# Optimization experiments

Hardware: AMD Instinct MI355X
Metric: run time of the kernel (lower is better)

## Reference

```python
import jax, jax.numpy as jnp
from jax import lax
import numpy as np

B, L, H, V = 256, 2048, 128, 32000
THR = 0.4      # energy_threshold
LN_EPS = 1e-5  # torch LayerNorm default


def setup_inputs() -> dict:
    key = jax.random.key(0)
    ks = jax.random.split(key, 12)
    s = lambda k, shp, scale: (jax.random.normal(k, shp, dtype=jnp.float32) * scale)
    return {
        "seq": jax.random.randint(ks[0], (B, L), 0, V),
        "embed": s(ks[1], (V, H), 0.02),
        "W1": s(ks[2], (H, 2 * H), H ** -0.5),
        "b1": jnp.zeros((2 * H,), jnp.float32),
        "W2": s(ks[3], (2 * H, H), (2 * H) ** -0.5),
        "b2": jnp.zeros((H,), jnp.float32),
        "gamma": jnp.ones((H,), jnp.float32),
        "beta": jnp.zeros((H,), jnp.float32),
        "Wrp": s(ks[4], (H, H), H ** -0.5),
        "brp": jnp.zeros((H,), jnp.float32),
        "Wout": s(ks[5], (H, V), H ** -0.5),
        "bout": jnp.zeros((V,), jnp.float32),
    }


def _encode(seq, embed, W1, b1, W2, b2, gamma, beta):
    e = embed[seq]                                         # [B,L,H]
    ff = jnp.maximum(e @ W1 + b1, 0.0) @ W2 + b2           # [B,L,H]
    y = e + ff
    mu = y.mean(-1, keepdims=True)
    var = ((y - mu) ** 2).mean(-1, keepdims=True)
    return (y - mu) * lax.rsqrt(var + LN_EPS) * gamma + beta


def reference(seq, embed, W1, b1, W2, b2, gamma, beta, Wrp, brp, Wout, bout):
    h_all = _encode(seq, embed, W1, b1, W2, b2, gamma, beta)  # [B,L,H]

    def step(M, k):
        # k = v = h_all[:, t, :]  -> [B,H]
        v = k
        vp = jnp.einsum('bij,bj->bi', M, k)
        error = v - vp / (jnp.sum(k * k, axis=-1, keepdims=True) + 1e-6)
        gate = (jnp.linalg.norm(error, axis=-1)
                > THR * jnp.linalg.norm(v, axis=-1)).astype(M.dtype)  # [B]
        M = M + gate[:, None, None] * jnp.einsum('bi,bj->bij', error, k)
        return M, None

    M0 = jnp.zeros((B, H, H), h_all.dtype)
    ks = jnp.swapaxes(h_all[:, :-1, :], 0, 1)               # [L-1,B,H]
    M_fin, _ = lax.scan(step, M0, ks)
    r = jnp.einsum('bij,bj->bi', M_fin, h_all[:, -1, :])    # [B,H]
    return (r @ Wrp + brp) @ Wout + bout                    # [B,V]
```

## Files before the change

kernel.cpp:

```cpp
#include <hip/hip_runtime.h>
#include <hip/hip_bf16.h>


#define BB 256
#define LL 2048
#define HH 128
#define VV 32000
#define RS 136

typedef float f32x2 __attribute__((ext_vector_type(2)));

__device__ __forceinline__ void dma16(const float* g, float* l) {
  __builtin_amdgcn_global_load_lds(
      (const __attribute__((address_space(1))) void*)g,
      (__attribute__((address_space(3))) void*)l,
      16, 0, 0);
}

template <int CTRL>
__device__ __forceinline__ float dppadd(float x) {
  int y = __builtin_amdgcn_update_dpp(0, __float_as_int(x), CTRL, 0xF, 0xF, true);
  return x + __int_as_float(y);
}

__device__ __forceinline__ void pkfma(f32x2& d, f32x2 a, f32x2 b) {
  asm("v_pk_fma_f32 %0, %1, %2, %0" : "+v"(d) : "v"(a), "v"(b));
}

__device__ __forceinline__ void barrier_lgkm() {
  asm volatile("s_waitcnt lgkmcnt(0)\n\ts_barrier" ::: "memory");
}
__device__ __forceinline__ void wait_vmN(int n) {
  if (n == 3)      asm volatile("s_waitcnt vmcnt(3)" ::: "memory");
  else if (n == 2) asm volatile("s_waitcnt vmcnt(2)" ::: "memory");
  else if (n == 1) asm volatile("s_waitcnt vmcnt(1)" ::: "memory");
  else             asm volatile("s_waitcnt vmcnt(0)" ::: "memory");
}

__global__ __launch_bounds__(256, 1) void build_htab_kernel(
    const float* __restrict__ embed,
    const float* __restrict__ W1,
    const float* __restrict__ b1,
    const float* __restrict__ W2,
    const float* __restrict__ b2,
    const float* __restrict__ gamma,
    const float* __restrict__ beta,
    float* __restrict__ Htab2)
{
  const int tid = threadIdx.x;
  const int j   = tid & 127;
  const int h2  = tid >> 7;

  float w1r[128];
#pragma unroll
  for (int m = 0; m < 128; ++m) w1r[m] = W1[m * 256 + tid];

  const float b1n = b1[tid];
  const float b2j = b2[j];
  const float gj  = gamma[j];
  const float bj  = beta[j];

  __shared__ __align__(16) float4 w2q[64][128];
  __shared__ __align__(16) float e_s[128];
  __shared__ __align__(16) float a_s[256];
  __shared__ float p_s[2][128];
  __shared__ float red[8];

  for (int idx = tid; idx < 8192; idx += 256) {
    int n4 = idx >> 7, jj = idx & 127;
    float4 w;
    w.x = W2[(size_t)(4 * n4 + 0) * 128 + jj];
    w.y = W2[(size_t)(4 * n4 + 1) * 128 + jj];
    w.z = W2[(size_t)(4 * n4 + 2) * 128 + jj];
    w.w = W2[(size_t)(4 * n4 + 3) * 128 + jj];
    w2q[n4][jj] = w;
  }
  __syncthreads();

  for (int v = blockIdx.x; v < VV; v += gridDim.x) {
    if (tid < 128) e_s[tid] = embed[(size_t)v * 128 + tid];
    __syncthreads();

    float acc[4] = {b1n, 0.f, 0.f, 0.f};
#pragma unroll
    for (int q = 0; q < 32; ++q) {
      float4 ev = *(const float4*)&e_s[4 * q];
      float t = ev.x * w1r[4 * q + 0];
      t = fmaf(ev.y, w1r[4 * q + 1], t);
      t = fmaf(ev.z, w1r[4 * q + 2], t);
      t = fmaf(ev.w, w1r[4 * q + 3], t);
      acc[q & 3] += t;
    }
    float a = fmaxf((acc[0] + acc[1]) + (acc[2] + acc[3]), 0.0f);
    a_s[tid] = a;
    __syncthreads();

    float p0 = 0.f, p1 = 0.f, p2v = 0.f, p3 = 0.f;
#pragma unroll
    for (int q = 0; q < 32; ++q) {
      int n4 = h2 * 32 + q;
      float4 av = *(const float4*)&a_s[4 * n4];
      float4 wq = w2q[n4][j];
      p0 = fmaf(av.x, wq.x, p0);
      p1 = fmaf(av.y, wq.y, p1);
      p2v = fmaf(av.z, wq.z, p2v);
      p3 = fmaf(av.w, wq.w, p3);
    }
    p_s[h2][j] = (p0 + p1) + (p2v + p3);
    __syncthreads();

    float y = 0.0f;
    if (tid < 128) {
      float ff = p_s[0][tid] + p_s[1][tid] + b2j;
      y = e_s[tid] + ff;
    }
    float s1 = y, s2 = y * y;
    s1 = dppadd<0xB1>(s1);  s2 = dppadd<0xB1>(s2);
    s1 = dppadd<0x4E>(s1);  s2 = dppadd<0x4E>(s2);
    s1 = dppadd<0x141>(s1); s2 = dppadd<0x141>(s2);
    s1 = dppadd<0x140>(s1); s2 = dppadd<0x140>(s2);
    s1 = dppadd<0x142>(s1); s2 = dppadd<0x142>(s2);
    s1 = dppadd<0x143>(s1); s2 = dppadd<0x143>(s2);
    if (tid < 128 && (tid & 63) == 63) {
      red[tid >> 6] = s1;
      red[2 + (tid >> 6)] = s2;
    }
    __syncthreads();
    float mu = (red[0] + red[1]) * (1.0f / 128.0f);
    float ms = (red[2] + red[3]) * (1.0f / 128.0f);
    float var = ms - mu * mu;
    float hv = 0.0f;
    if (tid < 128) {
      float dy = y - mu;
      hv = dy * (1.0f / sqrtf(var + 1e-5f)) * gj + bj;
      int ofs = tid + ((tid >> 6) << 2);
      Htab2[(size_t)v * RS + ofs] = hv;
    }
    float q2 = hv * hv;
    q2 = dppadd<0xB1>(q2);
    q2 = dppadd<0x4E>(q2);
    q2 = dppadd<0x141>(q2);
    q2 = dppadd<0x140>(q2);
    q2 = dppadd<0x142>(q2);
    q2 = dppadd<0x143>(q2);
    if (tid < 128 && (tid & 63) == 63) red[4 + (tid >> 6)] = q2;
    __syncthreads();
    if (tid == 0) {
      float kk = red[4] + red[5];
      Htab2[(size_t)v * RS + 132] = kk;
      Htab2[(size_t)v * RS + 133] = 1.0f / (kk + 1e-6f);
    }
    __syncthreads();
  }
}

__global__ __launch_bounds__(512, 2) void scan_kernel(
    const int* __restrict__ seq,
    const float* __restrict__ Htab2,
    const float* __restrict__ Wrp,
    const float* __restrict__ brp,
    float* __restrict__ rr)
{
  const int b     = blockIdx.x;
  const int tid   = threadIdx.x;
  const int i     = tid >> 2;
  const int q     = tid & 3;
  const int lane  = tid & 63;
  const int wv    = tid >> 6;
  const int iofs  = i + ((i >> 6) << 2);
  const int kbase = (q & 1) * 32 + (q >> 1) * 68;

  __shared__ int seq_s[LL];
  __shared__ __align__(16) float slots[8][RS];
  __shared__ __align__(16) float red_s[4][8];
  __shared__ __align__(16) float r_s[128];
  __shared__ float p2_s[4][128];

  {
    int t0 = seq[(size_t)b * LL + 0];
    int t1 = seq[(size_t)b * LL + 1];
    int t2 = seq[(size_t)b * LL + 2];
    int t3 = seq[(size_t)b * LL + 3];
    if (lane < 34) {
      dma16(Htab2 + (size_t)t0 * RS + lane * 4, &slots[0][0]);
      dma16(Htab2 + (size_t)t1 * RS + lane * 4, &slots[1][0]);
      dma16(Htab2 + (size_t)t2 * RS + lane * 4, &slots[2][0]);
      dma16(Htab2 + (size_t)t3 * RS + lane * 4, &slots[3][0]);
    }
  }
  for (int t = tid; t < LL; t += 512) seq_s[t] = seq[(size_t)b * LL + t];
  __syncthreads();

  f32x2 M2[16];
#pragma unroll
  for (int m = 0; m < 16; ++m) M2[m] = f32x2{0.f, 0.f};

  f32x2 kA[16], kB[16];
  float kiA, kkA, invA, kiB, kkB, invB;
  {
    const float4* kp = (const float4*)&slots[0][kbase];
#pragma unroll
    for (int m = 0; m < 8; ++m) {
      float4 tq = kp[m];
      kA[2 * m]     = f32x2{tq.x, tq.y};
      kA[2 * m + 1] = f32x2{tq.z, tq.w};
    }
    kiA = slots[0][iofs];
    float2 kv = *(const float2*)&slots[0][132];
    kkA = kv.x; invA = kv.y;
#pragma unroll
    for (int m = 0; m < 16; ++m) asm volatile("" : "+v"(kA[m]));
    asm volatile("" : "+v"(kiA), "+v"(kkA), "+v"(invA));
  }

  auto step = [&](f32x2 (&kc)[16], float ki_c, float kk_c, float inv_c,
                  f32x2 (&kn)[16], float& ki_n, float& kk_n, float& inv_n,
                  int t, int p, int sn, int sd, int nwait) {
    if (nwait == 3) {
      int tk = seq_s[t + 4];
      if (lane < 34)
        dma16(Htab2 + (size_t)tk * RS + lane * 4, &slots[sd][0]);
    }
    f32x2 a0{0.f,0.f}, a1{0.f,0.f}, a2{0.f,0.f}, a3{0.f,0.f};
#pragma unroll
    for (int m = 0; m < 4; ++m) {
      pkfma(a0, kc[4 * m + 0], M2[4 * m + 0]);
      pkfma(a1, kc[4 * m + 1], M2[4 * m + 1]);
      pkfma(a2, kc[4 * m + 2], M2[4 * m + 2]);
      pkfma(a3, kc[4 * m + 3], M2[4 * m + 3]);
    }
    float vp = ((a0.x + a0.y) + (a1.x + a1.y)) + ((a2.x + a2.y) + (a3.x + a3.y));
    vp = dppadd<0xB1>(vp);
    vp = dppadd<0x4E>(vp);
    float e = fmaf(-vp, inv_c, ki_c);
    float s = e * e;
    s = dppadd<0x141>(s);
    s = dppadd<0x140>(s);
    s = dppadd<0x142>(s);
    s = dppadd<0x143>(s);
    if (lane == 63) red_s[p][wv] = s;
    barrier_lgkm();

    float4 ra = *(const float4*)&red_s[p][0];
    float4 rb = *(const float4*)&red_s[p][4];
    wait_vmN(nwait);
    {
      const float4* kp = (const float4*)&slots[sn][kbase];
#pragma unroll
      for (int m = 0; m < 8; ++m) {
        float4 tq = kp[m];
        kn[2 * m]     = f32x2{tq.x, tq.y};
        kn[2 * m + 1] = f32x2{tq.z, tq.w};
      }
      ki_n = slots[sn][iofs];
      float2 kv = *(const float2*)&slots[sn][132];
      kk_n = kv.x; inv_n = kv.y;
    }
    float ne2 = ((ra.x + ra.y) + (ra.z + ra.w)) + ((rb.x + rb.y) + (rb.z + rb.w));
    float ge = (ne2 > 0.16f * kk_c) ? e : 0.0f;
    f32x2 ev{ge, ge};
#pragma unroll
    for (int m = 0; m < 16; ++m) pkfma(M2[m], ev, kc[m]);
#pragma unroll
    for (int m = 0; m < 16; ++m) asm volatile("" : "+v"(kn[m]));
    asm volatile("" : "+v"(ki_n), "+v"(kk_n), "+v"(inv_n));
  };

  for (int t = 0; t < 2040; t += 8) {
    step(kA, kiA, kkA, invA, kB, kiB, kkB, invB, t + 0, 0, 1, 4, 3);
    step(kB, kiB, kkB, invB, kA, kiA, kkA, invA, t + 1, 1, 2, 5, 3);
    step(kA, kiA, kkA, invA, kB, kiB, kkB, invB, t + 2, 2, 3, 6, 3);
    step(kB, kiB, kkB, invB, kA, kiA, kkA, invA, t + 3, 3, 4, 7, 3);
    step(kA, kiA, kkA, invA, kB, kiB, kkB, invB, t + 4, 0, 5, 0, 3);
    step(kB, kiB, kkB, invB, kA, kiA, kkA, invA, t + 5, 1, 6, 1, 3);
    step(kA, kiA, kkA, invA, kB, kiB, kkB, invB, t + 6, 2, 7, 2, 3);
    step(kB, kiB, kkB, invB, kA, kiA, kkA, invA, t + 7, 3, 0, 3, 3);
  }
  step(kA, kiA, kkA, invA, kB, kiB, kkB, invB, 2040, 0, 1, 4, 3);
  step(kB, kiB, kkB, invB, kA, kiA, kkA, invA, 2041, 1, 2, 5, 3);
  step(kA, kiA, kkA, invA, kB, kiB, kkB, invB, 2042, 2, 3, 6, 3);
  step(kB, kiB, kkB, invB, kA, kiA, kkA, invA, 2043, 3, 4, 7, 3);
  step(kA, kiA, kkA, invA, kB, kiB, kkB, invB, 2044, 0, 5, 0, 2);
  step(kB, kiB, kkB, invB, kA, kiA, kkA, invA, 2045, 1, 6, 1, 1);
  step(kA, kiA, kkA, invA, kB, kiB, kkB, invB, 2046, 2, 7, 2, 0);

  {
    f32x2 a0{0.f,0.f}, a1{0.f,0.f}, a2{0.f,0.f}, a3{0.f,0.f};
#pragma unroll
    for (int m = 0; m < 4; ++m) {
      pkfma(a0, kB[4 * m + 0], M2[4 * m + 0]);
      pkfma(a1, kB[4 * m + 1], M2[4 * m + 1]);
      pkfma(a2, kB[4 * m + 2], M2[4 * m + 2]);
      pkfma(a3, kB[4 * m + 3], M2[4 * m + 3]);
    }
    float vp = ((a0.x + a0.y) + (a1.x + a1.y)) + ((a2.x + a2.y) + (a3.x + a3.y));
    vp = dppadd<0xB1>(vp);
    vp = dppadd<0x4E>(vp);
    if (q == 0) r_s[i] = vp;
  }
  __syncthreads();

  const int j = tid & 127;
  const int g = tid >> 7;
  float pac[2] = {0.f, 0.f};
#pragma unroll
  for (int m = 0; m < 32; ++m) {
    pac[m & 1] = fmaf(r_s[g * 32 + m],
                      Wrp[(size_t)(g * 32 + m) * 128 + j], pac[m & 1]);
  }
  p2_s[g][j] = pac[0] + pac[1];
  __syncthreads();
  if (tid < 128) {
    rr[(size_t)b * 128 + tid] =
        p2_s[0][tid] + p2_s[1][tid] + p2_s[2][tid] + p2_s[3][tid] + brp[tid];
  }
}

__global__ __launch_bounds__(256, 1) void out_kernel(
    const float* __restrict__ rr,
    const float* __restrict__ Wout,
    const float* __restrict__ bout,
    float* __restrict__ out)
{
  const int tid = threadIdx.x;
  const int v = blockIdx.x * 64 + (tid & 63);
  const int bg = tid >> 6;
  const int b0 = blockIdx.y * 64;

  __shared__ float4 rs4[64][32];
  for (int idx = tid; idx < 2048; idx += 256) {
    int bb = idx >> 5, q = idx & 31;
    rs4[bb][q] = ((const float4*)rr)[(size_t)(b0 + bb) * 32 + q];
  }
  __syncthreads();

  float acc[16];
#pragma unroll
  for (int m = 0; m < 16; ++m) acc[m] = 0.0f;

  for (int h4 = 0; h4 < 32; ++h4) {
    float w0 = Wout[(size_t)(4 * h4 + 0) * VV + v];
    float w1 = Wout[(size_t)(4 * h4 + 1) * VV + v];
    float w2 = Wout[(size_t)(4 * h4 + 2) * VV + v];
    float w3 = Wout[(size_t)(4 * h4 + 3) * VV + v];
#pragma unroll
    for (int m = 0; m < 16; ++m) {
      float4 rv = rs4[bg * 16 + m][h4];
      float t = rv.x * w0;
      t = fmaf(rv.y, w1, t);
      t = fmaf(rv.z, w2, t);
      t = fmaf(rv.w, w3, t);
      acc[m] += t;
    }
  }
  float bo = bout[v];
#pragma unroll
  for (int m = 0; m < 16; ++m) {
    out[(size_t)(b0 + bg * 16 + m) * VV + v] = acc[m] + bo;
  }
}

extern "C" void kernel_launch(void* const* d_in, const int* in_sizes, int n_in,
                              void* d_out, int out_size, void* d_ws, size_t ws_size,
                              hipStream_t stream)
{
  const int* seq      = (const int*)d_in[0];
  const float* embed  = (const float*)d_in[1];
  const float* W1     = (const float*)d_in[2];
  const float* b1     = (const float*)d_in[3];
  const float* W2     = (const float*)d_in[4];
  const float* b2     = (const float*)d_in[5];
  const float* gamma  = (const float*)d_in[6];
  const float* beta   = (const float*)d_in[7];
  const float* Wrp    = (const float*)d_in[8];
  const float* brp    = (const float*)d_in[9];
  const float* Wout   = (const float*)d_in[10];
  const float* bout   = (const float*)d_in[11];
  float* out          = (float*)d_out;

  char* ws = (char*)d_ws;
  float* Htab2 = (float*)ws;
  float* rr    = (float*)(ws + 17408000);

  hipLaunchKernelGGL(build_htab_kernel, dim3(256), dim3(256), 0, stream,
                     embed, W1, b1, W2, b2, gamma, beta, Htab2);
  hipLaunchKernelGGL(scan_kernel, dim3(BB), dim3(512), 0, stream,
                     seq, Htab2, Wrp, brp, rr);
  hipLaunchKernelGGL(out_kernel, dim3(VV / 64, 4), dim3(256), 0, stream,
                     rr, Wout, bout, out);
}
```

Baseline: 1.456 ms.

## Software-pipeline scan recurrence with algebraic next-step correction to shorten critical path

Restructures the sequential memory-update scan so the M·k matvec for the next token is computed with the not-yet-updated M, then corrected by the rank-1 term (gate·e·(k_c·k_n)) using a cross-lane dot product reduced alongside the error norm. This removes the dependency of the next matvec on the current gated update, leaving one barrier per step on the critical path. It adds a third register key buffer, a deeper 6-slot prefetch with vmcnt(4), and reduced occupancy (launch bounds 512,1) to fit the extra registers. The reordering changes floating-point summation order and risks register pressure or spills.

After: 1.608 ms. 1.1x slower.

```diff
diff --git a/kernel.cpp b/kernel.cpp
--- a/kernel.cpp
+++ b/kernel.cpp
@@ -31,7 +31,9 @@
   asm volatile("s_waitcnt lgkmcnt(0)\n\ts_barrier" ::: "memory");
 }
 __device__ __forceinline__ void wait_vmN(int n) {
-  if (n == 3)      asm volatile("s_waitcnt vmcnt(3)" ::: "memory");
+  if (n == 5)      asm volatile("s_waitcnt vmcnt(5)" ::: "memory");
+  else if (n == 4) asm volatile("s_waitcnt vmcnt(4)" ::: "memory");
+  else if (n == 3) asm volatile("s_waitcnt vmcnt(3)" ::: "memory");
   else if (n == 2) asm volatile("s_waitcnt vmcnt(2)" ::: "memory");
   else if (n == 1) asm volatile("s_waitcnt vmcnt(1)" ::: "memory");
   else             asm volatile("s_waitcnt vmcnt(0)" ::: "memory");
@@ -154,7 +156,7 @@
   }
 }
 
-__global__ __launch_bounds__(512, 2) void scan_kernel(
+__global__ __launch_bounds__(512, 1) void scan_kernel(
     const int* __restrict__ seq,
     const float* __restrict__ Htab2,
     const float* __restrict__ Wrp,
@@ -171,21 +173,16 @@
   const int kbase = (q & 1) * 32 + (q >> 1) * 68;
 
   __shared__ int seq_s[LL];
-  __shared__ __align__(16) float slots[8][RS];
-  __shared__ __align__(16) float red_s[4][8];
+  __shared__ __align__(16) float slots[6][RS];
+  __shared__ __align__(16) float2 red2[3][8];
   __shared__ __align__(16) float r_s[128];
   __shared__ float p2_s[4][128];
 
   {
-    int t0 = seq[(size_t)b * LL + 0];
-    int t1 = seq[(size_t)b * LL + 1];
-    int t2 = seq[(size_t)b * LL + 2];
-    int t3 = seq[(size_t)b * LL + 3];
-    if (lane < 34) {
-      dma16(Htab2 + (size_t)t0 * RS + lane * 4, &slots[0][0]);
-      dma16(Htab2 + (size_t)t1 * RS + lane * 4, &slots[1][0]);
-      dma16(Htab2 + (size_t)t2 * RS + lane * 4, &slots[2][0]);
-      dma16(Htab2 + (size_t)t3 * RS + lane * 4, &slots[3][0]);
+    for (int jj = 0; jj < 6; ++jj) {
+      int tj = seq[(size_t)b * LL + jj];
+      if (lane < 34)
+        dma16(Htab2 + (size_t)tj * RS + lane * 4, &slots[jj][0]);
     }
   }
   for (int t = tid; t < LL; t += 512) seq_s[t] = seq[(size_t)b * LL + t];
@@ -195,8 +192,9 @@
 #pragma unroll
   for (int m = 0; m < 16; ++m) M2[m] = f32x2{0.f, 0.f};
 
-  f32x2 kA[16], kB[16];
+  f32x2 kA[16], kB[16], kC[16];
   float kiA, kkA, invA, kiB, kkB, invB;
+  float kiC = 0.f, kkC = 0.f, invC = 0.f;
   {
     const float4* kp = (const float4*)&slots[0][kbase];
 #pragma unroll
@@ -208,96 +206,117 @@
     kiA = slots[0][iofs];
     float2 kv = *(const float2*)&slots[0][132];
     kkA = kv.x; invA = kv.y;
-#pragma unroll
-    for (int m = 0; m < 16; ++m) asm volatile("" : "+v"(kA[m]));
-    asm volatile("" : "+v"(kiA), "+v"(kkA), "+v"(invA));
-  }
+  }
+  {
+    const float4* kp = (const float4*)&slots[1][kbase];
+#pragma unroll
+    for (int m = 0; m < 8; ++m) {
+      float4 tq = kp[m];
+      kB[2 * m]     = f32x2{tq.x, tq.y};
+      kB[2 * m + 1] = f32x2{tq.z, tq.w};
+    }
+    kiB = slots[1][iofs];
+    float2 kv = *(const float2*)&slots[1][132];
+    kkB = kv.x; invB = kv.y;
+  }
+#pragma unroll
+  for (int m = 0; m < 16; ++m) kC[m] = f32x2{0.f, 0.f};
+
+  __syncthreads();
+
+  float e   = kiA;
+  float vpb = 0.f;
+  int   tk  = seq_s[6];
 
   auto step = [&](f32x2 (&kc)[16], float ki_c, float kk_c, float inv_c,
-                  f32x2 (&kn)[16], float& ki_n, float& kk_n, float& inv_n,
-                  int t, int p, int sn, int sd, int nwait) {
-    if (nwait == 3) {
-      int tk = seq_s[t + 4];
+                  f32x2 (&kn)[16], float ki_n, float kk_n, float inv_n,
+                  f32x2 (&kr)[16], float& ki_r, float& kk_r, float& inv_r,
+                  int u, int p, int sn, int sd, int nwait,
+                  int do_issue, int do_pref, int do_refill, int do_tail) {
+    if (do_issue) {
       if (lane < 34)
         dma16(Htab2 + (size_t)tk * RS + lane * 4, &slots[sd][0]);
     }
-    f32x2 a0{0.f,0.f}, a1{0.f,0.f}, a2{0.f,0.f}, a3{0.f,0.f};
-#pragma unroll
-    for (int m = 0; m < 4; ++m) {
-      pkfma(a0, kc[4 * m + 0], M2[4 * m + 0]);
-      pkfma(a1, kc[4 * m + 1], M2[4 * m + 1]);
-      pkfma(a2, kc[4 * m + 2], M2[4 * m + 2]);
-      pkfma(a3, kc[4 * m + 3], M2[4 * m + 3]);
-    }
-    float vp = ((a0.x + a0.y) + (a1.x + a1.y)) + ((a2.x + a2.y) + (a3.x + a3.y));
-    vp = dppadd<0xB1>(vp);
-    vp = dppadd<0x4E>(vp);
-    float e = fmaf(-vp, inv_c, ki_c);
-    float s = e * e;
-    s = dppadd<0x141>(s);
-    s = dppadd<0x140>(s);
-    s = dppadd<0x142>(s);
-    s = dppadd<0x143>(s);
-    if (lane == 63) red_s[p][wv] = s;
+    float s  = e * e;
+    float c1 = ki_c * ki_n;
+    s = dppadd<0x141>(s);  c1 = dppadd<0x141>(c1);
+    s = dppadd<0x140>(s);  c1 = dppadd<0x140>(c1);
+    s = dppadd<0x142>(s);  c1 = dppadd<0x142>(c1);
+    s = dppadd<0x143>(s);  c1 = dppadd<0x143>(c1);
+    if (lane == 63) red2[p][wv] = float2{s, c1};
     barrier_lgkm();
 
-    float4 ra = *(const float4*)&red_s[p][0];
-    float4 rb = *(const float4*)&red_s[p][4];
-    wait_vmN(nwait);
-    {
+    const float4* rp = (const float4*)&red2[p][0];
+    float4 ra = rp[0], rb = rp[1], rc = rp[2], rd = rp[3];
+    if (do_refill) {
+      wait_vmN(nwait);
       const float4* kp = (const float4*)&slots[sn][kbase];
 #pragma unroll
       for (int m = 0; m < 8; ++m) {
         float4 tq = kp[m];
-        kn[2 * m]     = f32x2{tq.x, tq.y};
-        kn[2 * m + 1] = f32x2{tq.z, tq.w};
+        kr[2 * m]     = f32x2{tq.x, tq.y};
+        kr[2 * m + 1] = f32x2{tq.z, tq.w};
       }
-      ki_n = slots[sn][iofs];
+      ki_r = slots[sn][iofs];
       float2 kv = *(const float2*)&slots[sn][132];
-      kk_n = kv.x; inv_n = kv.y;
-    }
-    float ne2 = ((ra.x + ra.y) + (ra.z + ra.w)) + ((rb.x + rb.y) + (rb.z + rb.w));
-    float ge = (ne2 > 0.16f * kk_c) ? e : 0.0f;
-    f32x2 ev{ge, ge};
-#pragma unroll
-    for (int m = 0; m < 16; ++m) pkfma(M2[m], ev, kc[m]);
-#pragma unroll
-    for (int m = 0; m < 16; ++m) asm volatile("" : "+v"(kn[m]));
-    asm volatile("" : "+v"(ki_n), "+v"(kk_n), "+v"(inv_n));
+      kk_r = kv.x; inv_r = kv.y;
+    }
+    if (do_pref) tk = seq_s[u + 7];
+    float ne2 = ((ra.x + ra.z) + (rb.x + rb.z)) + ((rc.x + rc.z) + (rd.x + rd.z));
+    float cc  = ((ra.y + ra.w) + (rb.y + rb.w)) + ((rc.y + rc.w) + (rd.y + rd.w));
+    int  g  = ne2 > 0.16f * kk_c;
+    float ge = g ? e : 0.0f;
+    float ce = g ? cc : 0.0f;
+    float vp = fmaf(ce, e, vpb);
+    if (do_tail) { vpb = vp; return; }
+    e = fmaf(-vp, inv_n, ki_n);
+    f32x2 gev{ge, ge};
+#pragma unroll
+    for (int m = 0; m < 16; ++m) pkfma(M2[m], gev, kc[m]);
+    f32x2 a0{0.f,0.f}, a1{0.f,0.f}, a2{0.f,0.f}, a3{0.f,0.f};
+#pragma unroll
+    for (int m = 0; m < 4; ++m) {
+      pkfma(a0, kr[4 * m + 0], M2[4 * m + 0]);
+      pkfma(a1, kr[4 * m + 1], M2[4 * m + 1]);
+      pkfma(a2, kr[4 * m + 2], M2[4 * m + 2]);
+      pkfma(a3, kr[4 * m + 3], M2[4 * m + 3]);
+    }
+    float nv = ((a0.x + a0.y) + (a1.x + a1.y)) + ((a2.x + a2.y) + (a3.x + a3.y));
+    nv = dppadd<0xB1>(nv);
+    nv = dppadd<0x4E>(nv);
+    vpb = nv;
   };
 
-  for (int t = 0; t < 2040; t += 8) {
-    step(kA, kiA, kkA, invA, kB, kiB, kkB, invB, t + 0, 0, 1, 4, 3);
-    step(kB, kiB, kkB, invB, kA, kiA, kkA, invA, t + 1, 1, 2, 5, 3);
-    step(kA, kiA, kkA, invA, kB, kiB, kkB, invB, t + 2, 2, 3, 6, 3);
-    step(kB, kiB, kkB, invB, kA, kiA, kkA, invA, t + 3, 3, 4, 7, 3);
-    step(kA, kiA, kkA, invA, kB, kiB, kkB, invB, t + 4, 0, 5, 0, 3);
-    step(kB, kiB, kkB, invB, kA, kiA, kkA, invA, t + 5, 1, 6, 1, 3);
-    step(kA, kiA, kkA, invA, kB, kiB, kkB, invB, t + 6, 2, 7, 2, 3);
-    step(kB, kiB, kkB, invB, kA, kiA, kkA, invA, t + 7, 3, 0, 3, 3);
-  }
-  step(kA, kiA, kkA, invA, kB, kiB, kkB, invB, 2040, 0, 1, 4, 3);
-  step(kB, kiB, kkB, invB, kA, kiA, kkA, invA, 2041, 1, 2, 5, 3);
-  step(kA, kiA, kkA, invA, kB, kiB, kkB, invB, 2042, 2, 3, 6, 3);
-  step(kB, kiB, kkB, invB, kA, kiA, kkA, invA, 2043, 3, 4, 7, 3);
-  step(kA, kiA, kkA, invA, kB, kiB, kkB, invB, 2044, 0, 5, 0, 2);
-  step(kB, kiB, kkB, invB, kA, kiA, kkA, invA, 2045, 1, 6, 1, 1);
-  step(kA, kiA, kkA, invA, kB, kiB, kkB, invB, 2046, 2, 7, 2, 0);
-
-  {
-    f32x2 a0{0.f,0.f}, a1{0.f,0.f}, a2{0.f,0.f}, a3{0.f,0.f};
-#pragma unroll
-    for (int m = 0; m < 4; ++m) {
-      pkfma(a0, kB[4 * m + 0], M2[4 * m + 0]);
-      pkfma(a1, kB[4 * m + 1], M2[4 * m + 1]);
-      pkfma(a2, kB[4 * m + 2], M2[4 * m + 2]);
-      pkfma(a3, kB[4 * m + 3], M2[4 * m + 3]);
-    }
-    float vp = ((a0.x + a0.y) + (a1.x + a1.y)) + ((a2.x + a2.y) + (a3.x + a3.y));
-    vp = dppadd<0xB1>(vp);
-    vp = dppadd<0x4E>(vp);
-    if (q == 0) r_s[i] = vp;
-  }
+  for (int t = 0; t < 2040; t += 6) {
+    step(kA, kiA, kkA, invA, kB, kiB, kkB, invB, kC, kiC, kkC, invC,
+         t + 0, 0, 2, 0, 4, 1, 1, 1, 0);
+    step(kB, kiB, kkB, invB, kC, kiC, kkC, invC, kA, kiA, kkA, invA,
+         t + 1, 1, 3, 1, 4, 1, 1, 1, 0);
+    step(kC, kiC, kkC, invC, kA, kiA, kkA, invA, kB, kiB, kkB, invB,
+         t + 2, 2, 4, 2, 4, 1, 1, 1, 0);
+    step(kA, kiA, kkA, invA, kB, kiB, kkB, invB, kC, kiC, kkC, invC,
+         t + 3, 0, 5, 3, 4, 1, 1, 1, 0);
+    step(kB, kiB, kkB, invB, kC, kiC, kkC, invC, kA, kiA, kkA, invA,
+         t + 4, 1, 0, 4, 4, 1, 1, 1, 0);
+    step(kC, kiC, kkC, invC, kA, kiA, kkA, invA, kB, kiB, kkB, invB,
+         t + 5, 2, 1, 5, 4, 1, 1, 1, 0);
+  }
+  step(kA, kiA, kkA, invA, kB, kiB, kkB, invB, kC, kiC, kkC, invC,
+       2040, 0, 2, 0, 4, 1, 1, 1, 0);
+  step(kB, kiB, kkB, invB, kC, kiC, kkC, invC, kA, kiA, kkA, invA,
+       2041, 1, 3, 1, 4, 1, 0, 1, 0);
+  step(kC, kiC, kkC, invC, kA, kiA, kkA, invA, kB, kiB, kkB, invB,
+       2042, 2, 4, 2, 3, 0, 0, 1, 0);
+  step(kA, kiA, kkA, invA, kB, kiB, kkB, invB, kC, kiC, kkC, invC,
+       2043, 0, 5, 3, 2, 0, 0, 1, 0);
+  step(kB, kiB, kkB, invB, kC, kiC, kkC, invC, kA, kiA, kkA, invA,
+       2044, 1, 0, 4, 1, 0, 0, 1, 0);
+  step(kC, kiC, kkC, invC, kA, kiA, kkA, invA, kB, kiB, kkB, invB,
+       2045, 2, 1, 5, 0, 0, 0, 1, 0);
+  step(kA, kiA, kkA, invA, kB, kiB, kkB, invB, kC, kiC, kkC, invC,
+       2046, 0, 2, 0, 0, 0, 0, 0, 1);
+
+  if (q == 0) r_s[i] = vpb;
   __syncthreads();
 
   const int j = tid & 127;
```

## Retile scan state to 4x8 per-thread blocks of M with 16-lane row reductions

Applied to the files above, without the earlier changes.

Each thread now holds a 4-row by 8-column tile of the per-batch memory matrix instead of one row by 32 columns. This cuts per-thread k-vector registers and LDS reads (8 k values plus 4 ki values per step instead of 32 plus 1). In exchange, each row's matvec now needs a 16-lane DPP reduction done for four rows at once. Launch bounds change from 2 to 1 blocks per CU, which gives the compiler a larger register budget.

Result: no change. 1.460 ms (+0.2%).

```diff
diff --git a/kernel.cpp b/kernel.cpp
--- a/kernel.cpp
+++ b/kernel.cpp
@@ -154,7 +154,7 @@
   }
 }
 
-__global__ __launch_bounds__(512, 2) void scan_kernel(
+__global__ __launch_bounds__(512, 1) void scan_kernel(
     const int* __restrict__ seq,
     const float* __restrict__ Htab2,
     const float* __restrict__ Wrp,
@@ -163,12 +163,13 @@
 {
   const int b     = blockIdx.x;
   const int tid   = threadIdx.x;
-  const int i     = tid >> 2;
-  const int q     = tid & 3;
   const int lane  = tid & 63;
   const int wv    = tid >> 6;
-  const int iofs  = i + ((i >> 6) << 2);
-  const int kbase = (q & 1) * 32 + (q >> 1) * 68;
+  const int rg    = lane >> 4;
+  const int cg    = lane & 15;
+  const int i0    = wv * 16 + rg * 4;
+  const int iofs  = i0 + ((i0 >> 6) << 2);
+  const int kbase = (cg & 7) * 8 + (cg >> 3) * 68;
 
   __shared__ int seq_s[LL];
   __shared__ __align__(16) float slots[8][RS];
@@ -191,30 +192,29 @@
   for (int t = tid; t < LL; t += 512) seq_s[t] = seq[(size_t)b * LL + t];
   __syncthreads();
 
-  f32x2 M2[16];
-#pragma unroll
-  for (int m = 0; m < 16; ++m) M2[m] = f32x2{0.f, 0.f};
-
-  f32x2 kA[16], kB[16];
-  float kiA, kkA, invA, kiB, kkB, invB;
+  f32x2 M00{0.f,0.f}, M01{0.f,0.f}, M02{0.f,0.f}, M03{0.f,0.f};
+  f32x2 M10{0.f,0.f}, M11{0.f,0.f}, M12{0.f,0.f}, M13{0.f,0.f};
+  f32x2 M20{0.f,0.f}, M21{0.f,0.f}, M22{0.f,0.f}, M23{0.f,0.f};
+  f32x2 M30{0.f,0.f}, M31{0.f,0.f}, M32{0.f,0.f}, M33{0.f,0.f};
+
+  f32x2 kA0, kA1, kA2, kA3, kB0, kB1, kB2, kB3;
+  float4 kiA, kiB;
+  float kkA, invA, kkB, invB;
   {
-    const float4* kp = (const float4*)&slots[0][kbase];
-#pragma unroll
-    for (int m = 0; m < 8; ++m) {
-      float4 tq = kp[m];
-      kA[2 * m]     = f32x2{tq.x, tq.y};
-      kA[2 * m + 1] = f32x2{tq.z, tq.w};
-    }
-    kiA = slots[0][iofs];
+    const f32x2* kp = (const f32x2*)&slots[0][kbase];
+    kA0 = kp[0]; kA1 = kp[1]; kA2 = kp[2]; kA3 = kp[3];
+    kiA = *(const float4*)&slots[0][iofs];
     float2 kv = *(const float2*)&slots[0][132];
     kkA = kv.x; invA = kv.y;
-#pragma unroll
-    for (int m = 0; m < 16; ++m) asm volatile("" : "+v"(kA[m]));
-    asm volatile("" : "+v"(kiA), "+v"(kkA), "+v"(invA));
-  }
-
-  auto step = [&](f32x2 (&kc)[16], float ki_c, float kk_c, float inv_c,
-                  f32x2 (&kn)[16], float& ki_n, float& kk_n, float& inv_n,
+    asm volatile("" : "+v"(kA0), "+v"(kA1), "+v"(kA2), "+v"(kA3));
+    asm volatile("" : "+v"(kiA.x), "+v"(kiA.y), "+v"(kiA.z), "+v"(kiA.w));
+    asm volatile("" : "+v"(kkA), "+v"(invA));
+  }
+
+  auto step = [&](f32x2& kc0, f32x2& kc1, f32x2& kc2, f32x2& kc3,
+                  float4& kic, float kk_c, float inv_c,
+                  f32x2& kn0, f32x2& kn1, f32x2& kn2, f32x2& kn3,
+                  float4& kin, float& kk_n, float& inv_n,
                   int t, int p, int sn, int sd, int nwait) {
     if (nwait == 3) {
       int tk = seq_s[t + 4];
@@ -222,20 +222,25 @@
         dma16(Htab2 + (size_t)tk * RS + lane * 4, &slots[sd][0]);
     }
     f32x2 a0{0.f,0.f}, a1{0.f,0.f}, a2{0.f,0.f}, a3{0.f,0.f};
-#pragma unroll
-    for (int m = 0; m < 4; ++m) {
-      pkfma(a0, kc[4 * m + 0], M2[4 * m + 0]);
-      pkfma(a1, kc[4 * m + 1], M2[4 * m + 1]);
-      pkfma(a2, kc[4 * m + 2], M2[4 * m + 2]);
-      pkfma(a3, kc[4 * m + 3], M2[4 * m + 3]);
-    }
-    float vp = ((a0.x + a0.y) + (a1.x + a1.y)) + ((a2.x + a2.y) + (a3.x + a3.y));
-    vp = dppadd<0xB1>(vp);
-    vp = dppadd<0x4E>(vp);
-    float e = fmaf(-vp, inv_c, ki_c);
-    float s = e * e;
-    s = dppadd<0x141>(s);
-    s = dppadd<0x140>(s);
+    pkfma(a0, kc0, M00); pkfma(a0, kc1, M01); pkfma(a0, kc2, M02); pkfma(a0, kc3, M03);
+    pkfma(a1, kc0, M10); pkfma(a1, kc1, M11); pkfma(a1, kc2, M12); pkfma(a1, kc3, M13);
+    pkfma(a2, kc0, M20); pkfma(a2, kc1, M21); pkfma(a2, kc2, M22); pkfma(a2, kc3, M23);
+    pkfma(a3, kc0, M30); pkfma(a3, kc1, M31); pkfma(a3, kc2, M32); pkfma(a3, kc3, M33);
+    float v0 = a0.x + a0.y, v1 = a1.x + a1.y;
+    float v2 = a2.x + a2.y, v3 = a3.x + a3.y;
+    v0 = dppadd<0xB1>(v0);  v1 = dppadd<0xB1>(v1);
+    v2 = dppadd<0xB1>(v2);  v3 = dppadd<0xB1>(v3);
+    v0 = dppadd<0x4E>(v0);  v1 = dppadd<0x4E>(v1);
+    v2 = dppadd<0x4E>(v2);  v3 = dppadd<0x4E>(v3);
+    v0 = dppadd<0x141>(v0); v1 = dppadd<0x141>(v1);
+    v2 = dppadd<0x141>(v2); v3 = dppadd<0x141>(v3);
+    v0 = dppadd<0x140>(v0); v1 = dppadd<0x140>(v1);
+    v2 = dppadd<0x140>(v2); v3 = dppadd<0x140>(v3);
+    float e0 = fmaf(-v0, inv_c, kic.x);
+    float e1 = fmaf(-v1, inv_c, kic.y);
+    float e2 = fmaf(-v2, inv_c, kic.z);
+    float e3 = fmaf(-v3, inv_c, kic.w);
+    float s = fmaf(e3, e3, fmaf(e2, e2, fmaf(e1, e1, e0 * e0)));
     s = dppadd<0x142>(s);
     s = dppadd<0x143>(s);
     if (lane == 63) red_s[p][wv] = s;
@@ -245,58 +250,65 @@
     float4 rb = *(const float4*)&red_s[p][4];
     wait_vmN(nwait);
     {
-      const float4* kp = (const float4*)&slots[sn][kbase];
-#pragma unroll
-      for (int m = 0; m < 8; ++m) {
-        float4 tq = kp[m];
-        kn[2 * m]     = f32x2{tq.x, tq.y};
-        kn[2 * m + 1] = f32x2{tq.z, tq.w};
-      }
-      ki_n = slots[sn][iofs];
+      const f32x2* kp = (const f32x2*)&slots[sn][kbase];
+      kn0 = kp[0]; kn1 = kp[1]; kn2 = kp[2]; kn3 = kp[3];
+      kin = *(const float4*)&slots[sn][iofs];
       float2 kv = *(const float2*)&slots[sn][132];
       kk_n = kv.x; inv_n = kv.y;
     }
     float ne2 = ((ra.x + ra.y) + (ra.z + ra.w)) + ((rb.x + rb.y) + (rb.z + rb.w));
-    float ge = (ne2 > 0.16f * kk_c) ? e : 0.0f;
-    f32x2 ev{ge, ge};
-#pragma unroll
-    for (int m = 0; m < 16; ++m) pkfma(M2[m], ev, kc[m]);
-#pragma unroll
-    for (int m = 0; m < 16; ++m) asm volatile("" : "+v"(kn[m]));
-    asm volatile("" : "+v"(ki_n), "+v"(kk_n), "+v"(inv_n));
+    int g = ne2 > 0.16f * kk_c;
+    float ge0 = g ? e0 : 0.0f;
+    float ge1 = g ? e1 : 0.0f;
+    float ge2 = g ? e2 : 0.0f;
+    float ge3 = g ? e3 : 0.0f;
+    f32x2 g0{ge0, ge0}, g1{ge1, ge1}, g2{ge2, ge2}, g3{ge3, ge3};
+    pkfma(M00, g0, kc0); pkfma(M01, g0, kc1); pkfma(M02, g0, kc2); pkfma(M03, g0, kc3);
+    pkfma(M10, g1, kc0); pkfma(M11, g1, kc1); pkfma(M12, g1, kc2); pkfma(M13, g1, kc3);
+    pkfma(M20, g2, kc0); pkfma(M21, g2, kc1); pkfma(M22, g2, kc2); pkfma(M23, g2, kc3);
+    pkfma(M30, g3, kc0); pkfma(M31, g3, kc1); pkfma(M32, g3, kc2); pkfma(M33, g3, kc3);
+    asm volatile("" : "+v"(kn0), "+v"(kn1), "+v"(kn2), "+v"(kn3));
+    asm volatile("" : "+v"(kin.x), "+v"(kin.y), "+v"(kin.z), "+v"(kin.w));
+    asm volatile("" : "+v"(kk_n), "+v"(inv_n));
   };
 
   for (int t = 0; t < 2040; t += 8) {
-    step(kA, kiA, kkA, invA, kB, kiB, kkB, invB, t + 0, 0, 1, 4, 3);
-    step(kB, kiB, kkB, invB, kA, kiA, kkA, invA, t + 1, 1, 2, 5, 3);
-    step(kA, kiA, kkA, invA, kB, kiB, kkB, invB, t + 2, 2, 3, 6, 3);
-    step(kB, kiB, kkB, invB, kA, kiA, kkA, invA, t + 3, 3, 4, 7, 3);
-    step(kA, kiA, kkA, invA, kB, kiB, kkB, invB, t + 4, 0, 5, 0, 3);
-    step(kB, kiB, kkB, invB, kA, kiA, kkA, invA, t + 5, 1, 6, 1, 3);
-    step(kA, kiA, kkA, invA, kB, kiB, kkB, invB, t + 6, 2, 7, 2, 3);
-    step(kB, kiB, kkB, invB, kA, kiA, kkA, invA, t + 7, 3, 0, 3, 3);
-  }
-  step(kA, kiA, kkA, invA, kB, kiB, kkB, invB, 2040, 0, 1, 4, 3);
-  step(kB, kiB, kkB, invB, kA, kiA, kkA, invA, 2041, 1, 2, 5, 3);
-  step(kA, kiA, kkA, invA, kB, kiB, kkB, invB, 2042, 2, 3, 6, 3);
-  step(kB, kiB, kkB, invB, kA, kiA, kkA, invA, 2043, 3, 4, 7, 3);
-  step(kA, kiA, kkA, invA, kB, kiB, kkB, invB, 2044, 0, 5, 0, 2);
-  step(kB, kiB, kkB, invB, kA, kiA, kkA, invA, 2045, 1, 6, 1, 1);
-  step(kA, kiA, kkA, invA, kB, kiB, kkB, invB, 2046, 2, 7, 2, 0);
+    step(kA0,kA1,kA2,kA3, kiA, kkA, invA, kB0,kB1,kB2,kB3, kiB, kkB, invB, t + 0, 0, 1, 4, 3);
+    step(kB0,kB1,kB2,kB3, kiB, kkB, invB, kA0,kA1,kA2,kA3, kiA, kkA, invA, t + 1, 1, 2, 5, 3);
+    step(kA0,kA1,kA2,kA3, kiA, kkA, invA, kB0,kB1,kB2,kB3, kiB, kkB, invB, t + 2, 2, 3, 6, 3);
+    step(kB0,kB1,kB2,kB3, kiB, kkB, invB, kA0,kA1,kA2,kA3, kiA, kkA, invA, t + 3, 3, 4, 7, 3);
+    step(kA0,kA1,kA2,kA3, kiA, kkA, invA, kB0,kB1,kB2,kB3, kiB, kkB, invB, t + 4, 0, 5, 0, 3);
+    step(kB0,kB1,kB2,kB3, kiB, kkB, invB, kA0,kA1,kA2,kA3, kiA, kkA, invA, t + 5, 1, 6, 1, 3);
+    step(kA0,kA1,kA2,kA3, kiA, kkA, invA, kB0,kB1,kB2,kB3, kiB, kkB, invB, t + 6, 2, 7, 2, 3);
+    step(kB0,kB1,kB2,kB3, kiB, kkB, invB, kA0,kA1,kA2,kA3, kiA, kkA, invA, t + 7, 3, 0, 3, 3);
+  }
+  step(kA0,kA1,kA2,kA3, kiA, kkA, invA, kB0,kB1,kB2,kB3, kiB, kkB, invB, 2040, 0, 1, 4, 3);
+  step(kB0,kB1,kB2,kB3, kiB, kkB, invB, kA0,kA1,kA2,kA3, kiA, kkA, invA, 2041, 1, 2, 5, 3);
+  step(kA0,kA1,kA2,kA3, kiA, kkA, invA, kB0,kB1,kB2,kB3, kiB, kkB, invB, 2042, 2, 3, 6, 3);
+  step(kB0,kB1,kB2,kB3, kiB, kkB, invB, kA0,kA1,kA2,kA3, kiA, kkA, invA, 2043, 3, 4, 7, 3);
+  step(kA0,kA1,kA2,kA3, kiA, kkA, invA, kB0,kB1,kB2,kB3, kiB, kkB, invB, 2044, 0, 5, 0, 2);
+  step(kB0,kB1,kB2,kB3, kiB, kkB, invB, kA0,kA1,kA2,kA3, kiA, kkA, invA, 2045, 1, 6, 1, 1);
+  step(kA0,kA1,kA2,kA3, kiA, kkA, invA, kB0,kB1,kB2,kB3, kiB, kkB, invB, 2046, 2, 7, 2, 0);
 
   {
     f32x2 a0{0.f,0.f}, a1{0.f,0.f}, a2{0.f,0.f}, a3{0.f,0.f};
-#pragma unroll
-    for (int m = 0; m < 4; ++m) {
-      pkfma(a0, kB[4 * m + 0], M2[4 * m + 0]);
-      pkfma(a1, kB[4 * m + 1], M2[4 * m + 1]);
-      pkfma(a2, kB[4 * m + 2], M2[4 * m + 2]);
-      pkfma(a3, kB[4 * m + 3], M2[4 * m + 3]);
-    }
-    float vp = ((a0.x + a0.y) + (a1.x + a1.y)) + ((a2.x + a2.y) + (a3.x + a3.y));
-    vp = dppadd<0xB1>(vp);
-    vp = dppadd<0x4E>(vp);
-    if (q == 0) r_s[i] = vp;
+    pkfma(a0, kB0, M00); pkfma(a0, kB1, M01); pkfma(a0, kB2, M02); pkfma(a0, kB3, M03);
+    pkfma(a1, kB0, M10); pkfma(a1, kB1, M11); pkfma(a1, kB2, M12); pkfma(a1, kB3, M13);
+    pkfma(a2, kB0, M20); pkfma(a2, kB1, M21); pkfma(a2, kB2, M22); pkfma(a2, kB3, M23);
+    pkfma(a3, kB0, M30); pkfma(a3, kB1, M31); pkfma(a3, kB2, M32); pkfma(a3, kB3, M33);
+    float v0 = a0.x + a0.y, v1 = a1.x + a1.y;
+    float v2 = a2.x + a2.y, v3 = a3.x + a3.y;
+    v0 = dppadd<0xB1>(v0);  v1 = dppadd<0xB1>(v1);
+    v2 = dppadd<0xB1>(v2);  v3 = dppadd<0xB1>(v3);
+    v0 = dppadd<0x4E>(v0);  v1 = dppadd<0x4E>(v1);
+    v2 = dppadd<0x4E>(v2);  v3 = dppadd<0x4E>(v3);
+    v0 = dppadd<0x141>(v0); v1 = dppadd<0x141>(v1);
+    v2 = dppadd<0x141>(v2); v3 = dppadd<0x141>(v3);
+    v0 = dppadd<0x140>(v0); v1 = dppadd<0x140>(v1);
+    v2 = dppadd<0x140>(v2); v3 = dppadd<0x140>(v3);
+    if (cg == 0) {
+      *(float4*)&r_s[i0] = float4{v0, v1, v2, v3};
+    }
   }
   __syncthreads();
 
```
